# Kernel optimization log

Measured on AMD Instinct MI355X. Metric: run time of the kernel, lower is better.

The kernel has to match this reference:

```python
import jax, jax.numpy as jnp
import numpy as np

E = 1_000_000   # edges (temporal neighbor facts)
D = 128         # emb_dim
N = 200_000     # nodes carrying hidden state
B = 512         # queries (batch)
R = 240         # num_rel -> rel table has 2R+1 rows
T = 100_000     # tail nodes (scatter output size)


def setup_inputs() -> dict:
    key = jax.random.key(0)
    ks = jax.random.split(key, 14)
    b_col  = jax.random.randint(ks[0], (E,), 0, B)
    n_col  = jax.random.randint(ks[1], (E,), 0, N)
    h_col  = jax.random.randint(ks[2], (E,), 0, N)
    r_col  = jax.random.randint(ks[3], (E,), 0, 2 * R)   # r+1 in [1, 2R]
    t_col  = jax.random.randint(ks[4], (E,), 0, N)
    ts_col = jax.random.randint(ks[5], (E,), 0, 1000)
    facts = jnp.stack([b_col, n_col, h_col, r_col, t_col, ts_col], axis=1)
    s = 1.0 / np.sqrt(D)
    return {
        "hidden":     jax.random.normal(ks[6], (N, D), jnp.float32) * 0.02,
        "rel_table":  jax.random.normal(ks[7], (2 * R + 1, D), jnp.float32) * 0.02,
        "Ws":         jax.random.normal(ks[8], (D, D), jnp.float32) * s,
        "Wr":         jax.random.normal(ks[9], (D, D), jnp.float32) * s,
        "Wqr_w":      jax.random.normal(ks[10], (D, D), jnp.float32) * s,
        "Wqr_b":      jnp.zeros((D,), jnp.float32),
        "wa_w":       jax.random.normal(ks[11], (D, 1), jnp.float32) * s,
        "wa_b":       jnp.zeros((1,), jnp.float32),
        "Wh":         jax.random.normal(ks[12], (D, D), jnp.float32) * s,
        "query_rel":  jax.random.randint(ks[13], (B,), 0, 2 * R),
        "facts":      facts,
        "tail_index": jax.random.randint(jax.random.fold_in(key, 99), (E,), 0, T),
        "tail_nodes": jnp.arange(T),
    }


def reference(hidden, rel_table, Ws, Wr, Wqr_w, Wqr_b, wa_w, wa_b, Wh,
              query_rel, facts, tail_index, tail_nodes):
    b = facts[:, 0]
    n = facts[:, 1]
    r = facts[:, 3]
    h_e = hidden[n]                      # [E, D] gather node hidden
    hr  = rel_table[r + 1]               # [E, D] gather relation emb
    q_r = rel_table[query_rel + 1][b]    # [E, D] per-edge query relation
    # attention MLP: sigmoid(w_alpha(relu(Ws h + Wr r + Wqr q + b)))
    pre = h_e @ Ws + hr @ Wr + (q_r @ Wqr_w + Wqr_b)          # [E, D]
    alpha = jax.nn.sigmoid(jax.nn.relu(pre) @ wa_w + wa_b)    # [E, 1]
    message = alpha * (h_e + hr)                              # [E, D]
    agg = jax.ops.segment_sum(message, tail_index,
                              num_segments=tail_nodes.shape[0])  # [T, D]
    return agg @ Wh                      # act = identity (default)
```

## Files before the change

kernel.cpp:

```cpp
#include <hip/hip_runtime.h>
#include <hip/hip_fp16.h>
#include <math.h>

#define DD 128
#define CAP 64

typedef _Float16 half_t;
typedef __attribute__((ext_vector_type(8))) _Float16 half8;
typedef __attribute__((ext_vector_type(4))) float floatx4;

#define LDW 136

__device__ __forceinline__ __half2 relu2(__half2 x) {
    return __hmul2(x, __hgt2(x, __float2half2_rn(0.f)));
}

__global__ void wt4(const float* __restrict__ W0, const float* __restrict__ W1,
                    const float* __restrict__ W2, const float* __restrict__ W3,
                    half_t* __restrict__ T0, half_t* __restrict__ T1,
                    half_t* __restrict__ T2, half_t* __restrict__ T3) {
    const float* W = blockIdx.x == 0 ? W0 : blockIdx.x == 1 ? W1 : blockIdx.x == 2 ? W2 : W3;
    half_t* T      = blockIdx.x == 0 ? T0 : blockIdx.x == 1 ? T1 : blockIdx.x == 2 ? T2 : T3;
    for (int i = threadIdx.x; i < DD * DD; i += blockDim.x) {
        int n = i >> 7, k = i & 127;
        T[i] = (half_t)W[(size_t)k * DD + n];
    }
}

__global__ __launch_bounds__(256) void gemm_mfma(
    const float* __restrict__ table, const int* __restrict__ idx, int idxAdd, int M,
    const half_t* __restrict__ WT_g, const float* __restrict__ bias,
    float* __restrict__ OutF, __half* __restrict__ OutH) {
    __shared__ half_t WT[DD * LDW];
    __shared__ half_t As[64 * LDW];
    int tid = threadIdx.x;
    int lane = tid & 63;
    int w = tid >> 6;
    int rowf = lane & 15;
    int kgrp = (lane >> 4) * 8;

    for (int i = tid; i < 2048; i += 256) {
        int n = i >> 4, ch = i & 15;
        *(half8*)(WT + n * LDW + ch * 8) = *(const half8*)(WT_g + n * DD + ch * 8);
    }
    int tileM = blockIdx.x * 64;
    for (int i = tid; i < 2048; i += 256) {
        int row = i >> 5, c4 = i & 31;
        int gr = tileM + row;
        float4 v = make_float4(0.f, 0.f, 0.f, 0.f);
        if (gr < M) {
            int src = idx ? (idx[gr] + idxAdd) : gr;
            v = *(const float4*)(table + (size_t)src * DD + c4 * 4);
        }
        __half2 h01 = __floats2half2_rn(v.x, v.y);
        __half2 h23 = __floats2half2_rn(v.z, v.w);
        *(uint2*)(As + row * LDW + c4 * 4) = make_uint2(*(unsigned*)&h01, *(unsigned*)&h23);
    }
    __syncthreads();

    floatx4 acc[8];
#pragma unroll
    for (int t = 0; t < 8; t++) acc[t] = (floatx4){0.f, 0.f, 0.f, 0.f};
    const half_t* ap = As + (w * 16 + rowf) * LDW + kgrp;
    const half_t* bp0 = WT + rowf * LDW + kgrp;
#pragma unroll
    for (int kk = 0; kk < DD; kk += 32) {
        half8 a = *(const half8*)(ap + kk);
#pragma unroll
        for (int t = 0; t < 8; t++) {
            half8 b = *(const half8*)(bp0 + t * 16 * LDW + kk);
            acc[t] = __builtin_amdgcn_mfma_f32_16x16x32_f16(a, b, acc[t], 0, 0, 0);
        }
    }
    int orow = tileM + w * 16 + (lane >> 4) * 4;
#pragma unroll
    for (int t = 0; t < 8; t++) {
        int col = t * 16 + rowf;
        float bv = bias ? bias[col] : 0.f;
#pragma unroll
        for (int i = 0; i < 4; i++) {
            int gr = orow + i;
            if (gr < M) {
                float o = acc[t][i] + bv;
                if (OutF) OutF[(size_t)gr * DD + col] = o;
                if (OutH) OutH[(size_t)gr * DD + col] = __float2half(o);
            }
        }
    }
}

__global__ __launch_bounds__(256) void gemm_pack_mfma(
    const float* __restrict__ table, int M,
    const half_t* __restrict__ WT_g, __half* __restrict__ Packed) {
    __shared__ half_t WT[DD * LDW];
    __shared__ half_t As[64 * LDW];
    int tid = threadIdx.x;
    int lane = tid & 63;
    int w = tid >> 6;
    int rowf = lane & 15;
    int kgrp = (lane >> 4) * 8;

    for (int i = tid; i < 2048; i += 256) {
        int n = i >> 4, ch = i & 15;
        *(half8*)(WT + n * LDW + ch * 8) = *(const half8*)(WT_g + n * DD + ch * 8);
    }
    int tileM = blockIdx.x * 64;
    for (int i = tid; i < 2048; i += 256) {
        int row = i >> 5, c4 = i & 31;
        int gr = tileM + row;
        float4 v = make_float4(0.f, 0.f, 0.f, 0.f);
        if (gr < M) v = *(const float4*)(table + (size_t)gr * DD + c4 * 4);
        __half2 h01 = __floats2half2_rn(v.x, v.y);
        __half2 h23 = __floats2half2_rn(v.z, v.w);
        uint2 u = make_uint2(*(unsigned*)&h01, *(unsigned*)&h23);
        *(uint2*)(As + row * LDW + c4 * 4) = u;
        if (gr < M) *(uint2*)(Packed + (size_t)gr * 256 + c4 * 4) = u;
    }
    __syncthreads();

    floatx4 acc[8];
#pragma unroll
    for (int t = 0; t < 8; t++) acc[t] = (floatx4){0.f, 0.f, 0.f, 0.f};
    const half_t* ap = As + (w * 16 + rowf) * LDW + kgrp;
    const half_t* bp0 = WT + rowf * LDW + kgrp;
#pragma unroll
    for (int kk = 0; kk < DD; kk += 32) {
        half8 a = *(const half8*)(ap + kk);
#pragma unroll
        for (int t = 0; t < 8; t++) {
            half8 b = *(const half8*)(bp0 + t * 16 * LDW + kk);
            acc[t] = __builtin_amdgcn_mfma_f32_16x16x32_f16(a, b, acc[t], 0, 0, 0);
        }
    }
    int orow = tileM + w * 16 + (lane >> 4) * 4;
#pragma unroll
    for (int t = 0; t < 8; t++) {
        int col = t * 16 + rowf;
#pragma unroll
        for (int i = 0; i < 4; i++) {
            int gr = orow + i;
            if (gr < M) Packed[(size_t)gr * 256 + 128 + col] = __float2half(acc[t][i]);
        }
    }
}

__global__ void scatter_kernel(const int* __restrict__ facts, const int* __restrict__ tail,
                               int* __restrict__ cursor, int2* __restrict__ meta, int E) {
    int e = blockIdx.x * blockDim.x + threadIdx.x;
    if (e >= E) return;
    int b = facts[e * 6 + 0];
    int n = facts[e * 6 + 1];
    int r = facts[e * 6 + 3];
    int t = tail[e];
    int slot = atomicAdd(&cursor[t], 1);
    if (slot < CAP) meta[(size_t)t * CAP + slot] = make_int2(n, (r + 1) | (b << 16));
}

__global__ __launch_bounds__(256) void agg_fused3(
    const __half* __restrict__ HB, const __half* __restrict__ RB,
    const __half* __restrict__ QB, const float* __restrict__ wa,
    const float* __restrict__ wa_b, const int2* __restrict__ meta,
    const int* __restrict__ cursor, float* __restrict__ agg, int T) {
    int w = threadIdx.x >> 6;
    int lane = threadIdx.x & 63;
    int seg = blockIdx.x * 4 + w;
    if (seg >= T) return;
    int hf = lane >> 5;
    int c = (lane & 31) * 4;
    int hoff = hf * 128 + c;
    float4 wv = *(const float4*)(wa + c);
    __half2 wa2a = __halves2half2(__float2half(wv.x), __float2half(wv.y));
    __half2 wa2b = __halves2half2(__float2half(wv.z), __float2half(wv.w));
    float wb = wa_b[0];
    int cnt = cursor[seg];
    if (cnt > CAP) cnt = CAP;
    const int2* mp = meta + (size_t)seg * CAP;
    __half2 acc2a = __float2half2_rn(0.f);
    __half2 acc2b = __float2half2_rn(0.f);

#define FB(m)                                                                  \
    {                                                                          \
        int n_ = (m).x, r_ = (m).y & 0xFFFF, b_ = (m).y >> 16;                 \
        __half2 h2a = *(const __half2*)(HB + (size_t)n_ * 256 + hoff);         \
        __half2 h2b = *(const __half2*)(HB + (size_t)n_ * 256 + hoff + 2);     \
        __half2 r2a = *(const __half2*)(RB + (size_t)r_ * 256 + hoff);         \
        __half2 r2b = *(const __half2*)(RB + (size_t)r_ * 256 + hoff + 2);     \
        __half2 q2a = *(const __half2*)(QB + (size_t)b_ * DD + c);             \
        __half2 q2b = *(const __half2*)(QB + (size_t)b_ * DD + c + 2);         \
        __half2 s2a = __hadd2(h2a, r2a);                                       \
        __half2 s2b = __hadd2(h2b, r2b);                                       \
        __half2 p2a = relu2(__hadd2(s2a, q2a));                                \
        __half2 p2b = relu2(__hadd2(s2b, q2b));                                \
        __half2 t2 = __hfma2(p2a, wa2a, __hmul2(p2b, wa2b));                   \
        float t = __half2float(__low2half(t2)) + __half2float(__high2half(t2));\
        _Pragma("unroll")                                                      \
        for (int o = 1; o < 32; o <<= 1) t += __shfl_xor(t, o);                \
        float tu = __shfl_xor(t, 32);       \
        float al = 1.f / (1.f + __expf(-(tu + wb)));                           \
        __half2 al2 = __float2half2_rn(al);                                    \
        if (!hf) {                                                             \
            acc2a = __hfma2(al2, s2a, acc2a);                                  \
            acc2b = __hfma2(al2, s2b, acc2b);                                  \
        }                                                                      \
    }

    int i = 0;
    for (; i + 1 < cnt; i += 2) {
        int2 m0 = mp[i];
        int2 m1 = mp[i + 1];
        FB(m0);
        FB(m1);
    }
    if (i < cnt) {
        int2 m0 = mp[i];
        FB(m0);
    }
#undef FB

    if (!hf) {
        float4 o;
        o.x = __half2float(__low2half(acc2a));
        o.y = __half2float(__high2half(acc2a));
        o.z = __half2float(__low2half(acc2b));
        o.w = __half2float(__high2half(acc2b));
        *(float4*)(agg + (size_t)seg * DD + c) = o;
    }
}

extern "C" void kernel_launch(void* const* d_in, const int* in_sizes, int n_in,
                              void* d_out, int out_size, void* d_ws, size_t ws_size,
                              hipStream_t stream) {
    const float* hidden    = (const float*)d_in[0];
    const float* rel_table = (const float*)d_in[1];
    const float* Ws        = (const float*)d_in[2];
    const float* Wr        = (const float*)d_in[3];
    const float* Wqr_w     = (const float*)d_in[4];
    const float* Wqr_b     = (const float*)d_in[5];
    const float* wa_w      = (const float*)d_in[6];
    const float* wa_b      = (const float*)d_in[7];
    const float* Wh        = (const float*)d_in[8];
    const int* query_rel   = (const int*)d_in[9];
    const int* facts       = (const int*)d_in[10];
    const int* tail_index  = (const int*)d_in[11];

    int N     = in_sizes[0] / DD;
    int Rrows = in_sizes[1] / DD;
    int B     = in_sizes[9];
    int E     = in_sizes[11];
    int T     = in_sizes[12];

    char* ws = (char*)d_ws;
    size_t off = 0;
    auto alloc = [&](size_t bytes) -> void* {
        void* p = ws + off;
        off += (bytes + 255) & ~(size_t)255;
        return p;
    };
    __half* HB  = (__half*)alloc((size_t)N * 256 * 2);
    __half* RB  = (__half*)alloc((size_t)Rrows * 256 * 2);
    __half* QB  = (__half*)alloc((size_t)B * DD * 2);
    int* cursor = (int*)alloc((size_t)T * 4);
    int2* meta  = (int2*)alloc((size_t)T * CAP * 8);
    float* agg  = (float*)alloc((size_t)T * DD * 4);
    half_t* WsT  = (half_t*)alloc((size_t)DD * DD * 2);
    half_t* WrT  = (half_t*)alloc((size_t)DD * DD * 2);
    half_t* WqrT = (half_t*)alloc((size_t)DD * DD * 2);
    half_t* WhT  = (half_t*)alloc((size_t)DD * DD * 2);

    (void)hipMemsetAsync(cursor, 0, (size_t)T * 4, stream);

    wt4<<<4, 256, 0, stream>>>(Ws, Wr, Wqr_w, Wh, WsT, WrT, WqrT, WhT);

    gemm_pack_mfma<<<(N + 63) / 64, 256, 0, stream>>>(hidden, N, WsT, HB);
    gemm_pack_mfma<<<(Rrows + 63) / 64, 256, 0, stream>>>(rel_table, Rrows, WrT, RB);
    gemm_mfma<<<(B + 63) / 64, 256, 0, stream>>>(rel_table, query_rel, 1, B,
                                                 WqrT, Wqr_b, nullptr, QB);

    scatter_kernel<<<(E + 255) / 256, 256, 0, stream>>>(facts, tail_index, cursor, meta, E);

    agg_fused3<<<(T + 3) / 4, 256, 0, stream>>>(HB, RB, QB, wa_w, wa_b,
                                                meta, cursor, agg, T);

    gemm_mfma<<<(T + 63) / 64, 256, 0, stream>>>(agg, nullptr, 0, T, WhT, nullptr,
                                                 (float*)d_out, nullptr);
}
```

Before: 475.0 us.

## Split per-edge attention into a separate alpha kernel and slim the aggregation

Result: slower. 517.6 us (+9.0%).

```diff
diff --git a/kernel.cpp b/kernel.cpp
--- a/kernel.cpp
+++ b/kernel.cpp
@@ -13,6 +13,12 @@
 
 __device__ __forceinline__ __half2 relu2(__half2 x) {
     return __hmul2(x, __hgt2(x, __float2half2_rn(0.f)));
+}
+
+template <int CTRL>
+__device__ __forceinline__ float dpp_add(float x) {
+    int y = __builtin_amdgcn_update_dpp(0, __float_as_int(x), CTRL, 0xf, 0xf, true);
+    return x + __int_as_float(y);
 }
 
 __global__ void wt4(const float* __restrict__ W0, const float* __restrict__ W1,
@@ -144,64 +150,85 @@
     }
 }
 
+__global__ __launch_bounds__(256) void alpha_kernel(
+    const __half* __restrict__ HB, const __half* __restrict__ RB,
+    const __half* __restrict__ QB, const int* __restrict__ facts,
+    const float* __restrict__ wa, const float* __restrict__ wa_b,
+    __half* __restrict__ alphaH, int E) {
+    int tid = threadIdx.x;
+    int lane = tid & 63;
+    int wv = blockIdx.x * 4 + (tid >> 6);
+    int e = wv * 2 + (lane >> 5);
+    bool valid = e < E;
+    int ec = valid ? e : (E - 1);
+    int c = (lane & 31) * 4;
+
+    int2 bn = *(const int2*)(facts + ec * 6);
+    int r = facts[ec * 6 + 3];
+    int b_ = bn.x, n_ = bn.y;
+
+    uint2 hu = *(const uint2*)(HB + n_ * 256 + 128 + c);
+    uint2 ru = *(const uint2*)(RB + (r + 1) * 256 + 128 + c);
+    uint2 qu = *(const uint2*)(QB + b_ * DD + c);
+    __half2 h2a = *(__half2*)&hu.x, h2b = *(__half2*)&hu.y;
+    __half2 r2a = *(__half2*)&ru.x, r2b = *(__half2*)&ru.y;
+    __half2 q2a = *(__half2*)&qu.x, q2b = *(__half2*)&qu.y;
+
+    float4 wv4 = *(const float4*)(wa + c);
+    __half2 wa2a = __halves2half2(__float2half(wv4.x), __float2half(wv4.y));
+    __half2 wa2b = __halves2half2(__float2half(wv4.z), __float2half(wv4.w));
+
+    __half2 p2a = relu2(__hadd2(__hadd2(h2a, r2a), q2a));
+    __half2 p2b = relu2(__hadd2(__hadd2(h2b, r2b), q2b));
+    __half2 t2 = __hfma2(p2a, wa2a, __hmul2(p2b, wa2b));
+    float t = __half2float(__low2half(t2)) + __half2float(__high2half(t2));
+
+    t = dpp_add<0x111>(t);
+    t = dpp_add<0x112>(t);
+    t = dpp_add<0x114>(t);
+    t = dpp_add<0x118>(t);
+    t = dpp_add<0x142>(t);
+
+    float al = 1.f / (1.f + __expf(-(t + wa_b[0])));
+    if (((lane & 31) == 31) && valid) alphaH[e] = __float2half(al);
+}
+
 __global__ void scatter_kernel(const int* __restrict__ facts, const int* __restrict__ tail,
+                               const __half* __restrict__ alphaH,
                                int* __restrict__ cursor, int2* __restrict__ meta, int E) {
     int e = blockIdx.x * blockDim.x + threadIdx.x;
     if (e >= E) return;
-    int b = facts[e * 6 + 0];
     int n = facts[e * 6 + 1];
     int r = facts[e * 6 + 3];
     int t = tail[e];
+    unsigned ab = __half_as_ushort(alphaH[e]);
     int slot = atomicAdd(&cursor[t], 1);
-    if (slot < CAP) meta[(size_t)t * CAP + slot] = make_int2(n, (r + 1) | (b << 16));
-}
-
-__global__ __launch_bounds__(256) void agg_fused3(
+    if (slot < CAP) meta[(size_t)t * CAP + slot] = make_int2(n, (r + 1) | (int)(ab << 16));
+}
+
+__global__ __launch_bounds__(256) void agg_lite(
     const __half* __restrict__ HB, const __half* __restrict__ RB,
-    const __half* __restrict__ QB, const float* __restrict__ wa,
-    const float* __restrict__ wa_b, const int2* __restrict__ meta,
-    const int* __restrict__ cursor, float* __restrict__ agg, int T) {
+    const int2* __restrict__ meta, const int* __restrict__ cursor,
+    float* __restrict__ agg, int T) {
     int w = threadIdx.x >> 6;
     int lane = threadIdx.x & 63;
     int seg = blockIdx.x * 4 + w;
     if (seg >= T) return;
-    int hf = lane >> 5;
-    int c = (lane & 31) * 4;
-    int hoff = hf * 128 + c;
-    float4 wv = *(const float4*)(wa + c);
-    __half2 wa2a = __halves2half2(__float2half(wv.x), __float2half(wv.y));
-    __half2 wa2b = __halves2half2(__float2half(wv.z), __float2half(wv.w));
-    float wb = wa_b[0];
     int cnt = cursor[seg];
     if (cnt > CAP) cnt = CAP;
-    const int2* mp = meta + (size_t)seg * CAP;
-    __half2 acc2a = __float2half2_rn(0.f);
-    __half2 acc2b = __float2half2_rn(0.f);
+    const int2* mp = meta + seg * CAP;
+    int co = lane * 2;
+    __half2 acc = __float2half2_rn(0.f);
 
 #define FB(m)                                                                  \
     {                                                                          \
-        int n_ = (m).x, r_ = (m).y & 0xFFFF, b_ = (m).y >> 16;                 \
-        __half2 h2a = *(const __half2*)(HB + (size_t)n_ * 256 + hoff);         \
-        __half2 h2b = *(const __half2*)(HB + (size_t)n_ * 256 + hoff + 2);     \
-        __half2 r2a = *(const __half2*)(RB + (size_t)r_ * 256 + hoff);         \
-        __half2 r2b = *(const __half2*)(RB + (size_t)r_ * 256 + hoff + 2);     \
-        __half2 q2a = *(const __half2*)(QB + (size_t)b_ * DD + c);             \
-        __half2 q2b = *(const __half2*)(QB + (size_t)b_ * DD + c + 2);         \
-        __half2 s2a = __hadd2(h2a, r2a);                                       \
-        __half2 s2b = __hadd2(h2b, r2b);                                       \
-        __half2 p2a = relu2(__hadd2(s2a, q2a));                                \
-        __half2 p2b = relu2(__hadd2(s2b, q2b));                                \
-        __half2 t2 = __hfma2(p2a, wa2a, __hmul2(p2b, wa2b));                   \
-        float t = __half2float(__low2half(t2)) + __half2float(__high2half(t2));\
-        _Pragma("unroll")                                                      \
-        for (int o = 1; o < 32; o <<= 1) t += __shfl_xor(t, o);                \
-        float tu = __shfl_xor(t, 32);       \
-        float al = 1.f / (1.f + __expf(-(tu + wb)));                           \
-        __half2 al2 = __float2half2_rn(al);                                    \
-        if (!hf) {                                                             \
-            acc2a = __hfma2(al2, s2a, acc2a);                                  \
-            acc2b = __hfma2(al2, s2b, acc2b);                                  \
-        }                                                                      \
+        int n_ = (m).x;                                                        \
+        int rr = (m).y & 0xFFFF;                                               \
+        __half al = __ushort_as_half((unsigned short)((unsigned)(m).y >> 16)); \
+        unsigned hu = *(const unsigned*)(HB + n_ * 256 + co);                  \
+        unsigned ru = *(const unsigned*)(RB + rr * 256 + co);                  \
+        __half2 s = __hadd2(*(__half2*)&hu, *(__half2*)&ru);                   \
+        acc = __hfma2(__half2half2(al), s, acc);                               \
     }
 
     int i = 0;
@@ -217,14 +244,10 @@
     }
 #undef FB
 
-    if (!hf) {
-        float4 o;
-        o.x = __half2float(__low2half(acc2a));
-        o.y = __half2float(__high2half(acc2a));
-        o.z = __half2float(__low2half(acc2b));
-        o.w = __half2float(__high2half(acc2b));
-        *(float4*)(agg + (size_t)seg * DD + c) = o;
-    }
+    float2 o;
+    o.x = __half2float(__low2half(acc));
+    o.y = __half2float(__high2half(acc));
+    *(float2*)(agg + seg * DD + co) = o;
 }
 
 extern "C" void kernel_launch(void* const* d_in, const int* in_sizes, int n_in,
@@ -266,6 +289,7 @@
     half_t* WrT  = (half_t*)alloc((size_t)DD * DD * 2);
     half_t* WqrT = (half_t*)alloc((size_t)DD * DD * 2);
     half_t* WhT  = (half_t*)alloc((size_t)DD * DD * 2);
+    __half* alphaH = (__half*)alloc((size_t)E * 2);
 
     (void)hipMemsetAsync(cursor, 0, (size_t)T * 4, stream);
 
@@ -276,10 +300,13 @@
     gemm_mfma<<<(B + 63) / 64, 256, 0, stream>>>(rel_table, query_rel, 1, B,
                                                  WqrT, Wqr_b, nullptr, QB);
 
-    scatter_kernel<<<(E + 255) / 256, 256, 0, stream>>>(facts, tail_index, cursor, meta, E);
-
-    agg_fused3<<<(T + 3) / 4, 256, 0, stream>>>(HB, RB, QB, wa_w, wa_b,
-                                                meta, cursor, agg, T);
+    alpha_kernel<<<(E + 7) / 8, 256, 0, stream>>>(HB, RB, QB, facts, wa_w, wa_b,
+                                                  alphaH, E);
+
+    scatter_kernel<<<(E + 255) / 256, 256, 0, stream>>>(facts, tail_index, alphaH,
+                                                        cursor, meta, E);
+
+    agg_lite<<<(T + 3) / 4, 256, 0, stream>>>(HB, RB, meta, cursor, agg, T);
 
     gemm_mfma<<<(T + 63) / 64, 256, 0, stream>>>(agg, nullptr, 0, T, WhT, nullptr,
                                                  (float*)d_out, nullptr);
```

## Apply Wh projection before aggregation and drop the final output GEMM

Applied to the files above, without the earlier changes.

Result: no change. 465.7 us (-1.9%).

```diff
diff --git a/kernel.cpp b/kernel.cpp
--- a/kernel.cpp
+++ b/kernel.cpp
@@ -13,6 +13,12 @@
 
 __device__ __forceinline__ __half2 relu2(__half2 x) {
     return __hmul2(x, __hgt2(x, __float2half2_rn(0.f)));
+}
+
+template <int CTRL>
+__device__ __forceinline__ float dpp_add(float x) {
+    int y = __builtin_amdgcn_update_dpp(0, __float_as_int(x), CTRL, 0xf, 0xf, true);
+    return x + __int_as_float(y);
 }
 
 __global__ void wt4(const float* __restrict__ W0, const float* __restrict__ W1,
@@ -25,6 +31,93 @@
         int n = i >> 7, k = i & 127;
         T[i] = (half_t)W[(size_t)k * DD + n];
     }
+}
+
+__device__ __forceinline__ void mfma_pass(
+    const half_t* As, const half_t* WT, int w, int lane, floatx4 acc[8]) {
+    int rowf = lane & 15;
+    int kgrp = (lane >> 4) * 8;
+#pragma unroll
+    for (int t = 0; t < 8; t++) acc[t] = (floatx4){0.f, 0.f, 0.f, 0.f};
+    const half_t* ap = As + (w * 16 + rowf) * LDW + kgrp;
+    const half_t* bp0 = WT + rowf * LDW + kgrp;
+#pragma unroll
+    for (int kk = 0; kk < DD; kk += 32) {
+        half8 a = *(const half8*)(ap + kk);
+#pragma unroll
+        for (int t = 0; t < 8; t++) {
+            half8 b = *(const half8*)(bp0 + t * 16 * LDW + kk);
+            acc[t] = __builtin_amdgcn_mfma_f32_16x16x32_f16(a, b, acc[t], 0, 0, 0);
+        }
+    }
+}
+
+__device__ __forceinline__ void acc_to_lds(const floatx4 acc[8], half_t* OutT,
+                                           int w, int lane) {
+    int rowf = lane & 15;
+    int rbase = w * 16 + (lane >> 4) * 4;
+#pragma unroll
+    for (int t = 0; t < 8; t++) {
+        int col = t * 16 + rowf;
+#pragma unroll
+        for (int i = 0; i < 4; i++) OutT[(rbase + i) * LDW + col] = (half_t)acc[t][i];
+    }
+}
+
+__device__ __forceinline__ void lds_to_packed(const half_t* OutT, int tileM, int M,
+                                              int tid, __half* Packed, int halfOff) {
+    for (int ch = tid; ch < 1024; ch += 256) {
+        int row = ch >> 4, off = (ch & 15) * 8;
+        int gr = tileM + row;
+        if (gr < M) {
+            half8 v = *(const half8*)(OutT + row * LDW + off);
+            *(uint4*)(Packed + (size_t)gr * 256 + halfOff + off) = *(uint4*)&v;
+        }
+    }
+}
+
+__global__ __launch_bounds__(256) void gemm_pack2(
+    const float* __restrict__ table, int M,
+    const half_t* __restrict__ WT1_g, const half_t* __restrict__ WT2_g,
+    __half* __restrict__ Packed) {
+    __shared__ half_t WT[DD * LDW];
+    __shared__ half_t As[64 * LDW];
+    int tid = threadIdx.x;
+    int lane = tid & 63;
+    int w = tid >> 6;
+    int tileM = blockIdx.x * 64;
+
+    for (int i = tid; i < 2048; i += 256) {
+        int row = i >> 5, c4 = i & 31;
+        int gr = tileM + row;
+        float4 v = make_float4(0.f, 0.f, 0.f, 0.f);
+        if (gr < M) v = *(const float4*)(table + (size_t)gr * DD + c4 * 4);
+        __half2 h01 = __floats2half2_rn(v.x, v.y);
+        __half2 h23 = __floats2half2_rn(v.z, v.w);
+        *(uint2*)(As + row * LDW + c4 * 4) = make_uint2(*(unsigned*)&h01, *(unsigned*)&h23);
+    }
+    for (int i = tid; i < 2048; i += 256) {
+        int n = i >> 4, ch = i & 15;
+        *(half8*)(WT + n * LDW + ch * 8) = *(const half8*)(WT1_g + n * DD + ch * 8);
+    }
+    __syncthreads();
+    floatx4 acc[8];
+    mfma_pass(As, WT, w, lane, acc);
+    __syncthreads();
+    acc_to_lds(acc, WT, w, lane);
+    __syncthreads();
+    lds_to_packed(WT, tileM, M, tid, Packed, 0);
+    __syncthreads();
+    for (int i = tid; i < 2048; i += 256) {
+        int n = i >> 4, ch = i & 15;
+        *(half8*)(WT + n * LDW + ch * 8) = *(const half8*)(WT2_g + n * DD + ch * 8);
+    }
+    __syncthreads();
+    mfma_pass(As, WT, w, lane, acc);
+    __syncthreads();
+    acc_to_lds(acc, WT, w, lane);
+    __syncthreads();
+    lds_to_packed(WT, tileM, M, tid, Packed, 128);
 }
 
 __global__ __launch_bounds__(256) void gemm_mfma(
@@ -37,7 +130,6 @@
     int lane = tid & 63;
     int w = tid >> 6;
     int rowf = lane & 15;
-    int kgrp = (lane >> 4) * 8;
 
     for (int i = tid; i < 2048; i += 256) {
         int n = i >> 4, ch = i & 15;
@@ -59,19 +151,7 @@
     __syncthreads();
 
     floatx4 acc[8];
-#pragma unroll
-    for (int t = 0; t < 8; t++) acc[t] = (floatx4){0.f, 0.f, 0.f, 0.f};
-    const half_t* ap = As + (w * 16 + rowf) * LDW + kgrp;
-    const half_t* bp0 = WT + rowf * LDW + kgrp;
-#pragma unroll
-    for (int kk = 0; kk < DD; kk += 32) {
-        half8 a = *(const half8*)(ap + kk);
-#pragma unroll
-        for (int t = 0; t < 8; t++) {
-            half8 b = *(const half8*)(bp0 + t * 16 * LDW + kk);
-            acc[t] = __builtin_amdgcn_mfma_f32_16x16x32_f16(a, b, acc[t], 0, 0, 0);
-        }
-    }
+    mfma_pass(As, WT, w, lane, acc);
     int orow = tileM + w * 16 + (lane >> 4) * 4;
 #pragma unroll
     for (int t = 0; t < 8; t++) {
@@ -85,61 +165,6 @@
                 if (OutF) OutF[(size_t)gr * DD + col] = o;
                 if (OutH) OutH[(size_t)gr * DD + col] = __float2half(o);
             }
-        }
-    }
-}
-
-__global__ __launch_bounds__(256) void gemm_pack_mfma(
-    const float* __restrict__ table, int M,
-    const half_t* __restrict__ WT_g, __half* __restrict__ Packed) {
-    __shared__ half_t WT[DD * LDW];
-    __shared__ half_t As[64 * LDW];
-    int tid = threadIdx.x;
-    int lane = tid & 63;
-    int w = tid >> 6;
-    int rowf = lane & 15;
-    int kgrp = (lane >> 4) * 8;
-
-    for (int i = tid; i < 2048; i += 256) {
-        int n = i >> 4, ch = i & 15;
-        *(half8*)(WT + n * LDW + ch * 8) = *(const half8*)(WT_g + n * DD + ch * 8);
-    }
-    int tileM = blockIdx.x * 64;
-    for (int i = tid; i < 2048; i += 256) {
-        int row = i >> 5, c4 = i & 31;
-        int gr = tileM + row;
-        float4 v = make_float4(0.f, 0.f, 0.f, 0.f);
-        if (gr < M) v = *(const float4*)(table + (size_t)gr * DD + c4 * 4);
-        __half2 h01 = __floats2half2_rn(v.x, v.y);
-        __half2 h23 = __floats2half2_rn(v.z, v.w);
-        uint2 u = make_uint2(*(unsigned*)&h01, *(unsigned*)&h23);
-        *(uint2*)(As + row * LDW + c4 * 4) = u;
-        if (gr < M) *(uint2*)(Packed + (size_t)gr * 256 + c4 * 4) = u;
-    }
-    __syncthreads();
-
-    floatx4 acc[8];
-#pragma unroll
-    for (int t = 0; t < 8; t++) acc[t] = (floatx4){0.f, 0.f, 0.f, 0.f};
-    const half_t* ap = As + (w * 16 + rowf) * LDW + kgrp;
-    const half_t* bp0 = WT + rowf * LDW + kgrp;
-#pragma unroll
-    for (int kk = 0; kk < DD; kk += 32) {
-        half8 a = *(const half8*)(ap + kk);
-#pragma unroll
-        for (int t = 0; t < 8; t++) {
-            half8 b = *(const half8*)(bp0 + t * 16 * LDW + kk);
-            acc[t] = __builtin_amdgcn_mfma_f32_16x16x32_f16(a, b, acc[t], 0, 0, 0);
-        }
-    }
-    int orow = tileM + w * 16 + (lane >> 4) * 4;
-#pragma unroll
-    for (int t = 0; t < 8; t++) {
-        int col = t * 16 + rowf;
-#pragma unroll
-        for (int i = 0; i < 4; i++) {
-            int gr = orow + i;
-            if (gr < M) Packed[(size_t)gr * 256 + 128 + col] = __float2half(acc[t][i]);
         }
     }
 }
@@ -156,11 +181,11 @@
     if (slot < CAP) meta[(size_t)t * CAP + slot] = make_int2(n, (r + 1) | (b << 16));
 }
 
-__global__ __launch_bounds__(256) void agg_fused3(
+__global__ __launch_bounds__(256) void agg_fused(
     const __half* __restrict__ HB, const __half* __restrict__ RB,
     const __half* __restrict__ QB, const float* __restrict__ wa,
     const float* __restrict__ wa_b, const int2* __restrict__ meta,
-    const int* __restrict__ cursor, float* __restrict__ agg, int T) {
+    const int* __restrict__ cursor, float* __restrict__ out, int T) {
     int w = threadIdx.x >> 6;
     int lane = threadIdx.x & 63;
     int seg = blockIdx.x * 4 + w;
@@ -175,32 +200,34 @@
     int cnt = cursor[seg];
     if (cnt > CAP) cnt = CAP;
     const int2* mp = meta + (size_t)seg * CAP;
-    __half2 acc2a = __float2half2_rn(0.f);
-    __half2 acc2b = __float2half2_rn(0.f);
+    float a0 = 0.f, a1 = 0.f, a2 = 0.f, a3 = 0.f;
 
 #define FB(m)                                                                  \
     {                                                                          \
         int n_ = (m).x, r_ = (m).y & 0xFFFF, b_ = (m).y >> 16;                 \
-        __half2 h2a = *(const __half2*)(HB + (size_t)n_ * 256 + hoff);         \
-        __half2 h2b = *(const __half2*)(HB + (size_t)n_ * 256 + hoff + 2);     \
-        __half2 r2a = *(const __half2*)(RB + (size_t)r_ * 256 + hoff);         \
-        __half2 r2b = *(const __half2*)(RB + (size_t)r_ * 256 + hoff + 2);     \
-        __half2 q2a = *(const __half2*)(QB + (size_t)b_ * DD + c);             \
-        __half2 q2b = *(const __half2*)(QB + (size_t)b_ * DD + c + 2);         \
-        __half2 s2a = __hadd2(h2a, r2a);                                       \
-        __half2 s2b = __hadd2(h2b, r2b);                                       \
-        __half2 p2a = relu2(__hadd2(s2a, q2a));                                \
-        __half2 p2b = relu2(__hadd2(s2b, q2b));                                \
-        __half2 t2 = __hfma2(p2a, wa2a, __hmul2(p2b, wa2b));                   \
+        uint2 hu = *(const uint2*)(HB + (size_t)n_ * 256 + hoff);              \
+        uint2 ru = *(const uint2*)(RB + (size_t)r_ * 256 + hoff);              \
+        uint2 qu = *(const uint2*)(QB + (size_t)b_ * DD + c);                  \
+        __half2 s2a = __hadd2(*(__half2*)&hu.x, *(__half2*)&ru.x);             \
+        __half2 s2b = __hadd2(*(__half2*)&hu.y, *(__half2*)&ru.y);             \
+        __half2 p2a = relu2(__hadd2(s2a, *(__half2*)&qu.x));                   \
+        __half2 p2b = relu2(__hadd2(s2b, *(__half2*)&qu.y));                   \
+        __half2 t2 = __hfma2(p2b, wa2b, __hmul2(p2a, wa2a));                   \
         float t = __half2float(__low2half(t2)) + __half2float(__high2half(t2));\
-        _Pragma("unroll")                                                      \
-        for (int o = 1; o < 32; o <<= 1) t += __shfl_xor(t, o);                \
-        float tu = __shfl_xor(t, 32);       \
+        t = dpp_add<0x111>(t);                                                 \
+        t = dpp_add<0x112>(t);                                                 \
+        t = dpp_add<0x114>(t);                                                 \
+        t = dpp_add<0x118>(t);                                                 \
+        t = dpp_add<0x142>(t);            \
+        float tu = __shfl(t, 63);                                              \
         float al = 1.f / (1.f + __expf(-(tu + wb)));                           \
-        __half2 al2 = __float2half2_rn(al);                                    \
         if (!hf) {                                                             \
-            acc2a = __hfma2(al2, s2a, acc2a);                                  \
-            acc2b = __hfma2(al2, s2b, acc2b);                                  \
+            float2 fa = __half22float2(s2a);                                   \
+            float2 fb = __half22float2(s2b);                                   \
+            a0 = fmaf(al, fa.x, a0);                                           \
+            a1 = fmaf(al, fa.y, a1);                                           \
+            a2 = fmaf(al, fb.x, a2);                                           \
+            a3 = fmaf(al, fb.y, a3);                                           \
         }                                                                      \
     }
 
@@ -217,14 +244,7 @@
     }
 #undef FB
 
-    if (!hf) {
-        float4 o;
-        o.x = __half2float(__low2half(acc2a));
-        o.y = __half2float(__high2half(acc2a));
-        o.z = __half2float(__low2half(acc2b));
-        o.w = __half2float(__high2half(acc2b));
-        *(float4*)(agg + (size_t)seg * DD + c) = o;
-    }
+    if (!hf) *(float4*)(out + (size_t)seg * DD + c) = make_float4(a0, a1, a2, a3);
 }
 
 extern "C" void kernel_launch(void* const* d_in, const int* in_sizes, int n_in,
@@ -261,7 +281,6 @@
     __half* QB  = (__half*)alloc((size_t)B * DD * 2);
     int* cursor = (int*)alloc((size_t)T * 4);
     int2* meta  = (int2*)alloc((size_t)T * CAP * 8);
-    float* agg  = (float*)alloc((size_t)T * DD * 4);
     half_t* WsT  = (half_t*)alloc((size_t)DD * DD * 2);
     half_t* WrT  = (half_t*)alloc((size_t)DD * DD * 2);
     half_t* WqrT = (half_t*)alloc((size_t)DD * DD * 2);
@@ -271,16 +290,14 @@
 
     wt4<<<4, 256, 0, stream>>>(Ws, Wr, Wqr_w, Wh, WsT, WrT, WqrT, WhT);
 
-    gemm_pack_mfma<<<(N + 63) / 64, 256, 0, stream>>>(hidden, N, WsT, HB);
-    gemm_pack_mfma<<<(Rrows + 63) / 64, 256, 0, stream>>>(rel_table, Rrows, WrT, RB);
+    gemm_pack2<<<(N + 63) / 64, 256, 0, stream>>>(hidden, N, WhT, WsT, HB);
+    gemm_pack2<<<(Rrows + 63) / 64, 256, 0, stream>>>(rel_table, Rrows, WhT, WrT, RB);
     gemm_mfma<<<(B + 63) / 64, 256, 0, stream>>>(rel_table, query_rel, 1, B,
                                                  WqrT, Wqr_b, nullptr, QB);
 
-    scatter_kernel<<<(E + 255) / 256, 256, 0, stream>>>(facts, tail_index, cursor, meta, E);
-
-    agg_fused3<<<(T + 3) / 4, 256, 0, stream>>>(HB, RB, QB, wa_w, wa_b,
-                                                meta, cursor, agg, T);
-
-    gemm_mfma<<<(T + 63) / 64, 256, 0, stream>>>(agg, nullptr, 0, T, WhT, nullptr,
-                                                 (float*)d_out, nullptr);
-}
+    scatter_kernel<<<(E + 255) / 256, 256, 0, stream>>>(facts, tail_index,
+                                                        cursor, meta, E);
+
+    agg_fused<<<(T + 3) / 4, 256, 0, stream>>>(HB, RB, QB, wa_w, wa_b,
+                                               meta, cursor, (float*)d_out, T);
+}
```
